# Optimization experiments

Hardware: AMD Instinct MI355X
Metric: run time of the kernel (lower is better)

## Reference

```python
import jax, jax.numpy as jnp
import numpy as np

WS = 8
HEADS = 12


def _dwconv(x, w, b):
    # x: (N, C, H, W); w: (C, 1, 3, 3) depthwise, zero pad 1
    y = jax.lax.conv_general_dilated(
        x, w, window_strides=(1, 1), padding=((1, 1), (1, 1)),
        dimension_numbers=("NCHW", "OIHW", "NCHW"), feature_group_count=x.shape[1])
    return y + b[None, :, None, None]


def _sepconv(x, dw, db, pw, pb):
    y = _dwconv(x, dw, db)
    # pointwise 1x1 conv: (N,C,H,W) x (O,C) -> (N,O,H,W)
    return jnp.einsum("nchw,oc->nohw", y, pw) + pb[None, :, None, None]


def _rel_pos_index(ws):
    coords = np.stack(np.meshgrid(np.arange(ws), np.arange(ws), indexing="ij"))  # (2, ws, ws)
    cf = coords.reshape(2, -1)
    rel = cf[:, :, None] - cf[:, None, :]          # (2, ws*ws, ws*ws)
    rel = rel.transpose(1, 2, 0).copy()
    rel[..., 0] += ws - 1
    rel[..., 1] += ws - 1
    rel[..., 0] *= 2 * ws - 1
    return rel.sum(-1)                             # (ws*ws, ws*ws)


def setup_inputs() -> dict:
    key = jax.random.key(0)
    ks = jax.random.split(key, 16)
    B, T, C, H, W = 2, 1, 384, 192, 192
    s = 0.02
    inp = {
        "vid": jax.random.normal(ks[0], (B, T, C, H, W), jnp.float32),
        "qd_w": jax.random.normal(ks[1], (C, 1, 3, 3), jnp.float32) * s,
        "qd_b": jnp.zeros((C,), jnp.float32),
        "qp_w": jax.random.normal(ks[2], (C, C), jnp.float32) * s,
        "qp_b": jnp.zeros((C,), jnp.float32),
        "kd_w": jax.random.normal(ks[3], (C, 1, 3, 3), jnp.float32) * s,
        "kd_b": jnp.zeros((C,), jnp.float32),
        "kp_w": jax.random.normal(ks[4], (C, C), jnp.float32) * s,
        "kp_b": jnp.zeros((C,), jnp.float32),
        "vd_w": jax.random.normal(ks[5], (C, 1, 3, 3), jnp.float32) * s,
        "vd_b": jnp.zeros((C,), jnp.float32),
        "vp_w": jax.random.normal(ks[6], (C, C), jnp.float32) * s,
        "vp_b": jnp.zeros((C,), jnp.float32),
        "rpb_table": jax.random.normal(ks[7], ((2 * WS - 1) ** 2, HEADS), jnp.float32) * s,
        "proj_w": jax.random.normal(ks[8], (C, C), jnp.float32) * s,
        "proj_b": jnp.zeros((C,), jnp.float32),
    }
    return inp


def reference(vid, qd_w, qd_b, qp_w, qp_b, kd_w, kd_b, kp_w, kp_b,
              vd_w, vd_b, vp_w, vp_b, rpb_table, proj_w, proj_b):
    B, T, C, H, W = vid.shape
    heads, ws = HEADS, WS
    hd = C // heads
    scale = hd ** -0.5
    x = vid.reshape(B * T, C, H, W)

    q = _sepconv(x, qd_w, qd_b, qp_w, qp_b) * scale
    k = _sepconv(x, kd_w, kd_b, kp_w, kp_b)
    v = _sepconv(x, vd_w, vd_b, vp_w, vp_b)

    nh, nw = H // ws, W // ws

    def win(z):  # (N, C, H, W) -> (N*nh*nw, heads, ws*ws, hd)
        N = z.shape[0]
        z = z.reshape(N, heads, hd, nh, ws, nw, ws)
        z = z.transpose(0, 3, 5, 1, 4, 6, 2)  # N, nh, nw, heads, ws, ws, hd
        return z.reshape(N * nh * nw, heads, ws * ws, hd)

    qw, kw, vw = win(q), win(k), win(v)

    # product search within window (dists = q . k), rel-pos bias softmax
    attn = jnp.einsum("nhqd,nhkd->nhqk", qw, kw)
    rp_idx = _rel_pos_index(ws)  # static (64, 64)
    bias = rpb_table[rp_idx.reshape(-1)].reshape(ws * ws, ws * ws, heads)
    bias = bias.transpose(2, 0, 1)  # (heads, 64, 64)
    attn = jax.nn.softmax(attn + bias[None], axis=-1)

    # weighted patch sum (ps=1 -> pixels)
    out = jnp.einsum("nhqk,nhkd->nhqd", attn, vw)  # (N*nh*nw, heads, ws*ws, hd)

    # un-window, merge heads into (h c) channel order, then token projection
    out = out.reshape(B * T, nh, nw, heads, ws, ws, hd)
    out = out.transpose(0, 1, 4, 2, 5, 3, 6).reshape(B * T, H, W, heads * hd)
    out = out @ proj_w.T + proj_b

    # fold (ps=1, stride0=1): identity overlap-add, zvid == 1
    out = out.transpose(0, 3, 1, 2).reshape(B, T, C, H, W)
    return out
```

## Files before the change

kernel.cpp:

```cpp
#include <hip/hip_runtime.h>

#define CCH 384
#define HH 192
#define WWD 192
#define NIMG 2
#define HWP (HH * WWD)
#define PTOT (NIMG * HWP)
#define HEADS 12
#define HD 32
#define NWIN 24
#define WINS 576
#define EELEM ((size_t)NIMG * CCH * HWP)
#define WMAT 147456

typedef __attribute__((ext_vector_type(8))) short bh8;
typedef __attribute__((ext_vector_type(8))) unsigned short us8;
typedef __attribute__((ext_vector_type(4))) unsigned short us4;
typedef __attribute__((ext_vector_type(4))) float fx4;

__device__ __forceinline__ unsigned short f2bf(float f) {
    unsigned u = __float_as_uint(f);
    u += 0x7fffu + ((u >> 16) & 1u);
    return (unsigned short)(u >> 16);
}

__device__ __forceinline__ void gload16(const void* g, void* l) {
    __builtin_amdgcn_global_load_lds(
        (const __attribute__((address_space(1))) void*)g,
        (__attribute__((address_space(3))) void*)l, 16, 0, 0);
}

__global__ __launch_bounds__(256) void prep(
    const float* __restrict__ qp, const float* __restrict__ kp,
    const float* __restrict__ vp, const float* __restrict__ pj,
    const float* __restrict__ qd, const float* __restrict__ kd,
    const float* __restrict__ vd, const float* __restrict__ rpb,
    unsigned short* __restrict__ Wb, float* __restrict__ dwT,
    float* __restrict__ Bx)
{
    int bx = blockIdx.x;
    if (bx < 288) {
        int idx8 = (bx * 256 + threadIdx.x) * 8;
        int which = idx8 / WMAT;
        int loc = idx8 - which * WMAT;
        const float* s = (which == 0) ? qp : (which == 1) ? kp : (which == 2) ? vp : pj;
        float4 v0 = *(const float4*)(s + loc);
        float4 v1 = *(const float4*)(s + loc + 4);
        us8 ov;
        ov[0] = f2bf(v0.x); ov[1] = f2bf(v0.y); ov[2] = f2bf(v0.z); ov[3] = f2bf(v0.w);
        ov[4] = f2bf(v1.x); ov[5] = f2bf(v1.y); ov[6] = f2bf(v1.z); ov[7] = f2bf(v1.w);
        *(us8*)(Wb + idx8) = ov;
    } else if (bx < 329) {
        int idx = (bx - 288) * 256 + threadIdx.x;
        if (idx < 3 * 9 * CCH) {
            int ten = idx / (9 * CCH);
            int rem = idx - ten * (9 * CCH);
            int tap = rem / CCH;
            int c   = rem - tap * CCH;
            const float* s = (ten == 0) ? qd : (ten == 1) ? kd : vd;
            dwT[idx] = s[c * 9 + tap];
        }
    } else {
        int idx = (bx - 329) * 256 + threadIdx.x;
        int h  = idx >> 12;
        int tk = (idx >> 6) & 63;
        int tq = idx & 63;
        int dy = (tq >> 3) - (tk >> 3) + 7;
        int dx = (tq & 7) - (tk & 7) + 7;
        Bx[idx] = rpb[(dy * 15 + dx) * HEADS + h];
    }
}

__global__ __launch_bounds__(256) void dwgather(
    const float* __restrict__ x,
    const float* __restrict__ wt,
    const float* __restrict__ qb, const float* __restrict__ kb,
    const float* __restrict__ vb,
    unsigned short* __restrict__ oq, unsigned short* __restrict__ ok,
    unsigned short* __restrict__ ov)
{
    __shared__ float halo[32 * 121];

    int bid = blockIdx.x;
    int b = (bid & 7) * 1728 + (bid >> 3);
    int wtx  = b % 24;
    int rest = b / 24;
    int chv  = rest % 12;
    int nwy  = rest / 12;
    int wy   = nwy % 24;
    int n    = nwy / 24;

    int h0 = wy * 8, w0 = wtx * 8;
    int tid = threadIdx.x;
    int c   = tid & 31;
    int pxg = tid >> 5;
    int cg  = chv * 32 + c;
    int widx = n * WINS + wy * NWIN + wtx;

    const float* xbase = x + (size_t)n * CCH * HWP + (size_t)(chv * 32) * HWP;

    for (int j = tid; j < 960; j += 256) {
        int seg = j % 3;
        int t   = j / 3;
        int rr  = t % 10;
        int cc  = t / 10;
        int hr  = h0 - 1 + rr;
        int cb  = w0 - 2 + seg * 4;
        float4 val = make_float4(0.f, 0.f, 0.f, 0.f);
        if (hr >= 0 && hr < HH) {
            const float* p = xbase + (size_t)cc * HWP + (size_t)hr * WWD;
            if (cb >= 0 && cb + 4 <= WWD) {
                val = *(const float4*)(p + cb);
            } else {
                if (cb + 0 >= 0 && cb + 0 < WWD) val.x = p[cb + 0];
                if (cb + 1 >= 0 && cb + 1 < WWD) val.y = p[cb + 1];
                if (cb + 2 >= 0 && cb + 2 < WWD) val.z = p[cb + 2];
                if (cb + 3 >= 0 && cb + 3 < WWD) val.w = p[cb + 3];
            }
        }
        int hb = cc * 121 + rr * 12 + seg * 4;
        halo[hb + 0] = val.x;
        halo[hb + 1] = val.y;
        halo[hb + 2] = val.z;
        halo[hb + 3] = val.w;
    }

    float wq[9], wk[9], wv[9];
#pragma unroll
    for (int t = 0; t < 9; ++t) {
        wq[t] = wt[t * CCH + cg];
        wk[t] = wt[9 * CCH + t * CCH + cg];
        wv[t] = wt[18 * CCH + t * CCH + cg];
    }
    float bqv = qb[cg], bkv = kb[cg], bvv = vb[cg];

    __syncthreads();

    const int hbase = c * 121 + pxg * 12;
    float r0[10], r1[10], r2[10];
#pragma unroll
    for (int cc = 0; cc < 10; ++cc) r0[cc] = halo[hbase + cc + 1];
#pragma unroll
    for (int cc = 0; cc < 10; ++cc) r1[cc] = halo[hbase + 12 + cc + 1];
#pragma unroll
    for (int cc = 0; cc < 10; ++cc) r2[cc] = halo[hbase + 24 + cc + 1];

    size_t ob0 = ((size_t)widx * 64 + pxg * 8) * CCH + cg;

#pragma unroll
    for (int pc = 0; pc < 8; ++pc) {
        float sq = 0.f, sk = 0.f, sv = 0.f;
#pragma unroll
        for (int dc = 0; dc < 3; ++dc) {
            float x0 = r0[pc + dc], x1 = r1[pc + dc], x2 = r2[pc + dc];
            sq = fmaf(x0, wq[dc], sq);     sk = fmaf(x0, wk[dc], sk);     sv = fmaf(x0, wv[dc], sv);
            sq = fmaf(x1, wq[3 + dc], sq); sk = fmaf(x1, wk[3 + dc], sk); sv = fmaf(x1, wv[3 + dc], sv);
            sq = fmaf(x2, wq[6 + dc], sq); sk = fmaf(x2, wk[6 + dc], sk); sv = fmaf(x2, wv[6 + dc], sv);
        }
        size_t o = ob0 + (size_t)pc * CCH;
        oq[o] = f2bf(sq + bqv);
        ok[o] = f2bf(sk + bkv);
        ov[o] = f2bf(sv + bvv);
    }
}

__global__ __launch_bounds__(256) void qkv_gemm(
    const unsigned short* __restrict__ tr0, const unsigned short* __restrict__ tr1,
    const unsigned short* __restrict__ tr2, const unsigned short* __restrict__ Wball,
    const float* __restrict__ qpb, const float* __restrict__ kpb,
    const float* __restrict__ vpb, float scale,
    unsigned short* __restrict__ qo, unsigned short* __restrict__ ko,
    unsigned short* __restrict__ vo)
{
    __shared__ __align__(16) char smem[33792];
    typedef unsigned short (*tile3)[128][32];
    tile3 Wt = (tile3)smem;
    tile3 Yt = (tile3)(smem + 16384);
    typedef unsigned short (*tep_t)[132];
    tep_t T16 = (tep_t)smem;

    int z = blockIdx.z;
    const unsigned short* Y  = (z == 0) ? tr0 : (z == 1) ? tr1 : tr2;
    const unsigned short* Wb = Wball + (size_t)z * WMAT;
    const float* bias        = (z == 0) ? qpb : (z == 1) ? kpb : vpb;
    float sc                 = (z == 0) ? scale : 1.0f;
    unsigned short* outb     = (z == 0) ? qo : (z == 1) ? ko : vo;
    bool vmode = (z == 2);

    int tid = threadIdx.x;
    int pp0 = blockIdx.x * 128;
    int cm0 = blockIdx.y * 128;
    int lid = tid & 63, wid = tid >> 6;
    int wr = wid >> 1, wc = wid & 1;
    int li = lid & 15, g = lid >> 4;

    int srow = (lid >> 2);
    int scol = (lid & 3) * 8;

    fx4 acc[4][4];
#pragma unroll
    for (int i = 0; i < 4; ++i)
#pragma unroll
        for (int j = 0; j < 4; ++j) acc[i][j] = (fx4){0.f, 0.f, 0.f, 0.f};

    tile3 A3 = vmode ? Yt : Wt;
    tile3 B3 = vmode ? Wt : Yt;

    const unsigned short* Wg0 = Wb + (size_t)(cm0 + wid * 32 + srow) * CCH + scol;
    const unsigned short* Yg0 = Y  + (size_t)(pp0 + wid * 32 + srow) * CCH + scol;

#pragma unroll
    for (int qi = 0; qi < 2; ++qi) {
        gload16(Wg0 + (size_t)qi * 16 * CCH, &Wt[0][wid * 32 + qi * 16][0]);
        gload16(Yg0 + (size_t)qi * 16 * CCH, &Yt[0][wid * 32 + qi * 16][0]);
    }
    __syncthreads();

    for (int kt = 0; kt < 12; ++kt) {
        int cur = kt & 1;
        if (kt < 11) {
            int k1 = (kt + 1) * 32;
#pragma unroll
            for (int qi = 0; qi < 2; ++qi) {
                gload16(Wg0 + (size_t)qi * 16 * CCH + k1, &Wt[cur ^ 1][wid * 32 + qi * 16][0]);
                gload16(Yg0 + (size_t)qi * 16 * CCH + k1, &Yt[cur ^ 1][wid * 32 + qi * 16][0]);
            }
        }

        bh8 a[4], b[4];
#pragma unroll
        for (int mf = 0; mf < 4; ++mf)
            a[mf] = *(const bh8*)&A3[cur][wr * 64 + mf * 16 + li][g * 8];
#pragma unroll
        for (int nf = 0; nf < 4; ++nf)
            b[nf] = *(const bh8*)&B3[cur][wc * 64 + nf * 16 + li][g * 8];
#pragma unroll
        for (int mf = 0; mf < 4; ++mf)
#pragma unroll
            for (int nf = 0; nf < 4; ++nf)
                acc[mf][nf] = __builtin_amdgcn_mfma_f32_16x16x32_bf16(
                    a[mf], b[nf], acc[mf][nf], 0, 0, 0);

        __syncthreads();
    }

    if (!vmode) {
#pragma unroll
        for (int mf = 0; mf < 4; ++mf) {
            int cl = wr * 64 + mf * 16 + g * 4;
            float4 bv = *(const float4*)&bias[cm0 + cl];
#pragma unroll
            for (int nf = 0; nf < 4; ++nf) {
                int pl = wc * 64 + nf * 16 + li;
                us4 o;
                o[0] = f2bf((acc[mf][nf][0] + bv.x) * sc);
                o[1] = f2bf((acc[mf][nf][1] + bv.y) * sc);
                o[2] = f2bf((acc[mf][nf][2] + bv.z) * sc);
                o[3] = f2bf((acc[mf][nf][3] + bv.w) * sc);
                *(us4*)&T16[pl][cl] = o;
            }
        }
        __syncthreads();
#pragma unroll
        for (int it = 0; it < 8; ++it) {
            int row = it * 16 + wid * 4 + (lid >> 4);
            int col = (lid & 15) * 8;
            us8 vv = *(const us8*)&T16[row][col];
            *(us8*)(outb + (size_t)(pp0 + row) * CCH + cm0 + col) = vv;
        }
    } else {
#pragma unroll
        for (int nf = 0; nf < 4; ++nf) {
            int cl = wc * 64 + nf * 16 + li;
            float bv = bias[cm0 + cl];
#pragma unroll
            for (int mf = 0; mf < 4; ++mf) {
                int pl = wr * 64 + mf * 16 + g * 4;
                us4 o;
                o[0] = f2bf(acc[mf][nf][0] + bv);
                o[1] = f2bf(acc[mf][nf][1] + bv);
                o[2] = f2bf(acc[mf][nf][2] + bv);
                o[3] = f2bf(acc[mf][nf][3] + bv);
                *(us4*)&T16[cl][pl] = o;
            }
        }
        __syncthreads();
        int n = pp0 / HWP;
        int pl0 = pp0 - n * HWP;
#pragma unroll
        for (int it = 0; it < 8; ++it) {
            int row = it * 16 + wid * 4 + (lid >> 4);
            int col = (lid & 15) * 8;
            us8 vv = *(const us8*)&T16[row][col];
            *(us8*)(outb + (size_t)(n * CCH + cm0 + row) * HWP + pl0 + col) = vv;
        }
    }
}

__global__ __launch_bounds__(256) void proj_gemm(
    const unsigned short* __restrict__ Y, const unsigned short* __restrict__ Wb,
    const float* __restrict__ bias, float* __restrict__ outf)
{
    __shared__ unsigned short Wt[2][128][32];
    __shared__ unsigned short Yt[2][128][32];

    int tid = threadIdx.x;
    int pp0 = blockIdx.x * 128;
    int cm0 = blockIdx.y * 128;
    int lid = tid & 63, wid = tid >> 6;
    int wr = wid >> 1, wc = wid & 1;
    int li = lid & 15, g = lid >> 4;

    int srow = (lid >> 2);
    int scol = (lid & 3) * 8;

    fx4 acc[4][4];
#pragma unroll
    for (int i = 0; i < 4; ++i)
#pragma unroll
        for (int j = 0; j < 4; ++j) acc[i][j] = (fx4){0.f, 0.f, 0.f, 0.f};

    const unsigned short* Wg0 = Wb + (size_t)(cm0 + wid * 32 + srow) * CCH + scol;
    const unsigned short* Yg0 = Y  + (size_t)(pp0 + wid * 32 + srow) * CCH + scol;

#pragma unroll
    for (int qi = 0; qi < 2; ++qi) {
        gload16(Wg0 + (size_t)qi * 16 * CCH, &Wt[0][wid * 32 + qi * 16][0]);
        gload16(Yg0 + (size_t)qi * 16 * CCH, &Yt[0][wid * 32 + qi * 16][0]);
    }
    __syncthreads();

    for (int kt = 0; kt < 12; ++kt) {
        int cur = kt & 1;
        if (kt < 11) {
            int k1 = (kt + 1) * 32;
#pragma unroll
            for (int qi = 0; qi < 2; ++qi) {
                gload16(Wg0 + (size_t)qi * 16 * CCH + k1, &Wt[cur ^ 1][wid * 32 + qi * 16][0]);
                gload16(Yg0 + (size_t)qi * 16 * CCH + k1, &Yt[cur ^ 1][wid * 32 + qi * 16][0]);
            }
        }

        bh8 a[4], b[4];
#pragma unroll
        for (int mf = 0; mf < 4; ++mf)
            a[mf] = *(const bh8*)&Wt[cur][wr * 64 + mf * 16 + li][g * 8];
#pragma unroll
        for (int nf = 0; nf < 4; ++nf)
            b[nf] = *(const bh8*)&Yt[cur][wc * 64 + nf * 16 + li][g * 8];
#pragma unroll
        for (int mf = 0; mf < 4; ++mf)
#pragma unroll
            for (int nf = 0; nf < 4; ++nf)
                acc[mf][nf] = __builtin_amdgcn_mfma_f32_16x16x32_bf16(
                    a[mf], b[nf], acc[mf][nf], 0, 0, 0);

        __syncthreads();
    }

#pragma unroll
    for (int mf = 0; mf < 4; ++mf) {
        int c = cm0 + wr * 64 + mf * 16 + g * 4;
#pragma unroll
        for (int nf = 0; nf < 4; ++nf) {
            int p = pp0 + wc * 64 + nf * 16 + li;
            int n = p / HWP;
            int rem = p - n * HWP;
            int win = rem >> 6, t = rem & 63;
            int h = (win / NWIN) * 8 + (t >> 3);
            int w = (win % NWIN) * 8 + (t & 7);
            float* op = outf + (size_t)n * CCH * HWP + (size_t)h * WWD + w;
#pragma unroll
            for (int r = 0; r < 4; ++r)
                op[(size_t)(c + r) * HWP] = acc[mf][nf][r] + bias[c + r];
        }
    }
}

__global__ __launch_bounds__(256) void attn(
    const unsigned short* __restrict__ q, const unsigned short* __restrict__ k,
    const unsigned short* __restrict__ v, const float* __restrict__ Bx,
    unsigned short* __restrict__ o)
{
    __shared__ unsigned short Pl[4][64][72];

    int tid = threadIdx.x, lid = tid & 63, wid = tid >> 6;
    int wl = blockIdx.x;
    int n = wl / WINS, winl = wl - n * WINS;
    int li = lid & 15, g = lid >> 4;

    const fx4 z = (fx4){0.f, 0.f, 0.f, 0.f};

    for (int hq = wid; hq < HEADS; hq += 4) {
        const unsigned short* qp = q + (size_t)(wl * 64) * CCH + hq * HD + g * 8;
        const unsigned short* kp = k + (size_t)(wl * 64) * CCH + hq * HD + g * 8;
        bh8 aq[4], bk[4];
#pragma unroll
        for (int mf = 0; mf < 4; ++mf)
            aq[mf] = *(const bh8*)(qp + (size_t)(mf * 16 + li) * CCH);
#pragma unroll
        for (int nf = 0; nf < 4; ++nf)
            bk[nf] = *(const bh8*)(kp + (size_t)(nf * 16 + li) * CCH);

        fx4 s[4][4];
#pragma unroll
        for (int mf = 0; mf < 4; ++mf)
#pragma unroll
            for (int nf = 0; nf < 4; ++nf)
                s[mf][nf] = __builtin_amdgcn_mfma_f32_16x16x32_bf16(aq[mf], bk[nf], z, 0, 0, 0);

#pragma unroll
        for (int mf = 0; mf < 4; ++mf)
#pragma unroll
            for (int nf = 0; nf < 4; ++nf) {
                fx4 bv = *(const fx4*)&Bx[((size_t)hq * 64 + nf * 16 + li) * 64
                                          + mf * 16 + g * 4];
                s[mf][nf] += bv;
            }

        float inv_[4][4];
#pragma unroll
        for (int mf = 0; mf < 4; ++mf)
#pragma unroll
            for (int r = 0; r < 4; ++r) {
                float m = s[mf][0][r];
#pragma unroll
                for (int nf = 1; nf < 4; ++nf) m = fmaxf(m, s[mf][nf][r]);
                m = fmaxf(m, __shfl_xor(m, 1));
                m = fmaxf(m, __shfl_xor(m, 2));
                m = fmaxf(m, __shfl_xor(m, 4));
                m = fmaxf(m, __shfl_xor(m, 8));
                float sum = 0.f;
#pragma unroll
                for (int nf = 0; nf < 4; ++nf) {
                    float e = __expf(s[mf][nf][r] - m);
                    s[mf][nf][r] = e;
                    sum += e;
                }
                sum += __shfl_xor(sum, 1);
                sum += __shfl_xor(sum, 2);
                sum += __shfl_xor(sum, 4);
                sum += __shfl_xor(sum, 8);
                inv_[mf][r] = 1.f / sum;
            }

#pragma unroll
        for (int mf = 0; mf < 4; ++mf)
#pragma unroll
            for (int nf = 0; nf < 4; ++nf)
#pragma unroll
                for (int r = 0; r < 4; ++r)
                    Pl[wid][mf * 16 + g * 4 + r][nf * 16 + li] =
                        f2bf(s[mf][nf][r] * inv_[mf][r]);

        fx4 o2[2][4];
#pragma unroll
        for (int m2 = 0; m2 < 2; ++m2)
#pragma unroll
            for (int nf = 0; nf < 4; ++nf) o2[m2][nf] = z;
#pragma unroll
        for (int ks = 0; ks < 2; ++ks) {
            bh8 av[2], bp[4];
#pragma unroll
            for (int m2 = 0; m2 < 2; ++m2)
                av[m2] = *(const bh8*)(v + (size_t)(n * CCH + hq * HD + m2 * 16 + li) * HWP
                                         + winl * 64 + ks * 32 + g * 8);
#pragma unroll
            for (int nf = 0; nf < 4; ++nf)
                bp[nf] = *(const bh8*)&Pl[wid][nf * 16 + li][ks * 32 + g * 8];
#pragma unroll
            for (int m2 = 0; m2 < 2; ++m2)
#pragma unroll
                for (int nf = 0; nf < 4; ++nf)
                    o2[m2][nf] = __builtin_amdgcn_mfma_f32_16x16x32_bf16(
                        av[m2], bp[nf], o2[m2][nf], 0, 0, 0);
        }
#pragma unroll
        for (int nf = 0; nf < 4; ++nf) {
            int tq = nf * 16 + li;
#pragma unroll
            for (int m2 = 0; m2 < 2; ++m2) {
                int d = hq * HD + m2 * 16 + g * 4;
                us4 ov;
                ov[0] = f2bf(o2[m2][nf][0]);
                ov[1] = f2bf(o2[m2][nf][1]);
                ov[2] = f2bf(o2[m2][nf][2]);
                ov[3] = f2bf(o2[m2][nf][3]);
                *(us4*)(o + (size_t)(wl * 64 + tq) * CCH + d) = ov;
            }
        }
    }
}

extern "C" void kernel_launch(void* const* d_in, const int* in_sizes, int n_in,
                              void* d_out, int out_size, void* d_ws, size_t ws_size,
                              hipStream_t stream) {
    const float* vid  = (const float*)d_in[0];
    const float* qd_w = (const float*)d_in[1];
    const float* qd_b = (const float*)d_in[2];
    const float* qp_w = (const float*)d_in[3];
    const float* qp_b = (const float*)d_in[4];
    const float* kd_w = (const float*)d_in[5];
    const float* kd_b = (const float*)d_in[6];
    const float* kp_w = (const float*)d_in[7];
    const float* kp_b = (const float*)d_in[8];
    const float* vd_w = (const float*)d_in[9];
    const float* vd_b = (const float*)d_in[10];
    const float* vp_w = (const float*)d_in[11];
    const float* vp_b = (const float*)d_in[12];
    const float* rpb  = (const float*)d_in[13];
    const float* pj_w = (const float*)d_in[14];
    const float* pj_b = (const float*)d_in[15];

    unsigned short* ws16 = (unsigned short*)d_ws;
    unsigned short* tr0 = ws16 + 3 * EELEM;
    unsigned short* tr1 = ws16 + 4 * EELEM;
    unsigned short* tr2 = ws16 + 5 * EELEM;
    unsigned short* Wb  = ws16 + 6 * EELEM;
    float* dwT          = (float*)(Wb + 4 * WMAT);
    float* Bx           = dwT + 3 * 9 * CCH;
    unsigned short* qb  = ws16;
    unsigned short* kb  = ws16 + EELEM;
    unsigned short* vb  = ws16 + 2 * EELEM;
    unsigned short* ob  = tr0;

    prep<<<521, 256, 0, stream>>>(qp_w, kp_w, vp_w, pj_w,
                                  qd_w, kd_w, vd_w, rpb, Wb, dwT, Bx);
    dwgather<<<NIMG * WINS * 12, 256, 0, stream>>>(
        vid, dwT, qd_b, kd_b, vd_b, tr0, tr1, tr2);

    const float scale = 0.17677669529663687f;
    qkv_gemm<<<dim3(PTOT / 128, 3, 3), 256, 0, stream>>>(
        tr0, tr1, tr2, Wb, qp_b, kp_b, vp_b, scale, qb, kb, vb);

    attn<<<NIMG * WINS, 256, 0, stream>>>(qb, kb, vb, Bx, ob);

    proj_gemm<<<dim3(PTOT / 128, 3), 256, 0, stream>>>(
        ob, Wb + 3 * WMAT, pj_b, (float*)d_out);
}
```

Baseline: 420.6 us.

## Widen dwconv tiles to 64 channels and swizzle GEMM LDS with XCD-aware block order

The depthwise-conv gather kernel now handles 64 channels per block and two pixel rows per thread. It reuses the loaded halo rows for the second row, which halves the block count and cuts redundant LDS reads. The QKV and projection GEMMs move to a 1D grid with a block-index remap that interleaves blocks across the 8 XCDs. They also XOR-swizzle the LDS column layout to reduce bank conflicts on MFMA fragment loads. The larger halo buffer raises LDS use per block, and the remap changes L2 locality in ways that are hard to predict.

```diff
diff --git a/kernel.cpp b/kernel.cpp
--- a/kernel.cpp
+++ b/kernel.cpp
@@ -79,27 +79,27 @@
     unsigned short* __restrict__ oq, unsigned short* __restrict__ ok,
     unsigned short* __restrict__ ov)
 {
-    __shared__ float halo[32 * 121];
+    __shared__ float halo[64 * 121];
 
     int bid = blockIdx.x;
-    int b = (bid & 7) * 1728 + (bid >> 3);
+    int b = (bid & 7) * 864 + (bid >> 3);
     int wtx  = b % 24;
-    int rest = b / 24;
-    int chv  = rest % 12;
-    int nwy  = rest / 12;
+    int strip = b / 24;
+    int chv  = strip % 6;
+    int nwy  = strip / 6;
     int wy   = nwy % 24;
     int n    = nwy / 24;
 
     int h0 = wy * 8, w0 = wtx * 8;
     int tid = threadIdx.x;
-    int c   = tid & 31;
-    int pxg = tid >> 5;
-    int cg  = chv * 32 + c;
+    int c   = tid & 63;
+    int pxg = tid >> 6;
+    int cg  = chv * 64 + c;
     int widx = n * WINS + wy * NWIN + wtx;
 
-    const float* xbase = x + (size_t)n * CCH * HWP + (size_t)(chv * 32) * HWP;
-
-    for (int j = tid; j < 960; j += 256) {
+    const float* xbase = x + (size_t)n * CCH * HWP + (size_t)(chv * 64) * HWP;
+
+    for (int j = tid; j < 1920; j += 256) {
         int seg = j % 3;
         int t   = j / 3;
         int rr  = t % 10;
@@ -136,7 +136,7 @@
 
     __syncthreads();
 
-    const int hbase = c * 121 + pxg * 12;
+    const int hbase = c * 121 + (2 * pxg) * 12;
     float r0[10], r1[10], r2[10];
 #pragma unroll
     for (int cc = 0; cc < 10; ++cc) r0[cc] = halo[hbase + cc + 1];
@@ -145,7 +145,7 @@
 #pragma unroll
     for (int cc = 0; cc < 10; ++cc) r2[cc] = halo[hbase + 24 + cc + 1];
 
-    size_t ob0 = ((size_t)widx * 64 + pxg * 8) * CCH + cg;
+    size_t ob0 = ((size_t)widx * 64 + pxg * 16) * CCH + cg;
 
 #pragma unroll
     for (int pc = 0; pc < 8; ++pc) {
@@ -158,6 +158,25 @@
             sq = fmaf(x2, wq[6 + dc], sq); sk = fmaf(x2, wk[6 + dc], sk); sv = fmaf(x2, wv[6 + dc], sv);
         }
         size_t o = ob0 + (size_t)pc * CCH;
+        oq[o] = f2bf(sq + bqv);
+        ok[o] = f2bf(sk + bkv);
+        ov[o] = f2bf(sv + bvv);
+    }
+
+#pragma unroll
+    for (int cc = 0; cc < 10; ++cc) r0[cc] = halo[hbase + 36 + cc + 1];
+
+#pragma unroll
+    for (int pc = 0; pc < 8; ++pc) {
+        float sq = 0.f, sk = 0.f, sv = 0.f;
+#pragma unroll
+        for (int dc = 0; dc < 3; ++dc) {
+            float x0 = r1[pc + dc], x1 = r2[pc + dc], x2 = r0[pc + dc];
+            sq = fmaf(x0, wq[dc], sq);     sk = fmaf(x0, wk[dc], sk);     sv = fmaf(x0, wv[dc], sv);
+            sq = fmaf(x1, wq[3 + dc], sq); sk = fmaf(x1, wk[3 + dc], sk); sv = fmaf(x1, wv[3 + dc], sv);
+            sq = fmaf(x2, wq[6 + dc], sq); sk = fmaf(x2, wk[6 + dc], sk); sv = fmaf(x2, wv[6 + dc], sv);
+        }
+        size_t o = ob0 + (size_t)(8 + pc) * CCH;
         oq[o] = f2bf(sq + bqv);
         ok[o] = f2bf(sk + bkv);
         ov[o] = f2bf(sv + bvv);
@@ -179,7 +198,14 @@
     typedef unsigned short (*tep_t)[132];
     tep_t T16 = (tep_t)smem;
 
-    int z = blockIdx.z;
+    int bL = blockIdx.x;
+    int O  = (bL & 7) * 648 + (bL >> 3);
+    int z  = O / 1728;
+    int rem = O - z * 1728;
+    int py = rem / 3;
+    int cx = rem - py * 3;
+    int pp0 = py * 128, cm0 = cx * 128;
+
     const unsigned short* Y  = (z == 0) ? tr0 : (z == 1) ? tr1 : tr2;
     const unsigned short* Wb = Wball + (size_t)z * WMAT;
     const float* bias        = (z == 0) ? qpb : (z == 1) ? kpb : vpb;
@@ -188,14 +214,13 @@
     bool vmode = (z == 2);
 
     int tid = threadIdx.x;
-    int pp0 = blockIdx.x * 128;
-    int cm0 = blockIdx.y * 128;
     int lid = tid & 63, wid = tid >> 6;
     int wr = wid >> 1, wc = wid & 1;
     int li = lid & 15, g = lid >> 4;
 
     int srow = (lid >> 2);
-    int scol = (lid & 3) * 8;
+    int scol = (((lid & 3) ^ ((srow >> 1) & 3))) * 8;
+    int gsw = (g ^ ((li >> 1) & 3)) * 8;
 
     fx4 acc[4][4];
 #pragma unroll
@@ -230,10 +255,10 @@
         bh8 a[4], b[4];
 #pragma unroll
         for (int mf = 0; mf < 4; ++mf)
-            a[mf] = *(const bh8*)&A3[cur][wr * 64 + mf * 16 + li][g * 8];
+            a[mf] = *(const bh8*)&A3[cur][wr * 64 + mf * 16 + li][gsw];
 #pragma unroll
         for (int nf = 0; nf < 4; ++nf)
-            b[nf] = *(const bh8*)&B3[cur][wc * 64 + nf * 16 + li][g * 8];
+            b[nf] = *(const bh8*)&B3[cur][wc * 64 + nf * 16 + li][gsw];
 #pragma unroll
         for (int mf = 0; mf < 4; ++mf)
 #pragma unroll
@@ -304,15 +329,20 @@
     __shared__ unsigned short Wt[2][128][32];
     __shared__ unsigned short Yt[2][128][32];
 
+    int bL = blockIdx.x;
+    int O  = (bL & 7) * 216 + (bL >> 3);
+    int py = O / 3;
+    int cx = O - py * 3;
+    int pp0 = py * 128, cm0 = cx * 128;
+
     int tid = threadIdx.x;
-    int pp0 = blockIdx.x * 128;
-    int cm0 = blockIdx.y * 128;
     int lid = tid & 63, wid = tid >> 6;
     int wr = wid >> 1, wc = wid & 1;
     int li = lid & 15, g = lid >> 4;
 
     int srow = (lid >> 2);
-    int scol = (lid & 3) * 8;
+    int scol = (((lid & 3) ^ ((srow >> 1) & 3))) * 8;
+    int gsw = (g ^ ((li >> 1) & 3)) * 8;
 
     fx4 acc[4][4];
 #pragma unroll
@@ -344,10 +374,10 @@
         bh8 a[4], b[4];
 #pragma unroll
         for (int mf = 0; mf < 4; ++mf)
-            a[mf] = *(const bh8*)&Wt[cur][wr * 64 + mf * 16 + li][g * 8];
+            a[mf] = *(const bh8*)&Wt[cur][wr * 64 + mf * 16 + li][gsw];
 #pragma unroll
         for (int nf = 0; nf < 4; ++nf)
-            b[nf] = *(const bh8*)&Yt[cur][wc * 64 + nf * 16 + li][g * 8];
+            b[nf] = *(const bh8*)&Yt[cur][wc * 64 + nf * 16 + li][gsw];
 #pragma unroll
         for (int mf = 0; mf < 4; ++mf)
 #pragma unroll
@@ -526,15 +556,15 @@
 
     prep<<<521, 256, 0, stream>>>(qp_w, kp_w, vp_w, pj_w,
                                   qd_w, kd_w, vd_w, rpb, Wb, dwT, Bx);
-    dwgather<<<NIMG * WINS * 12, 256, 0, stream>>>(
+    dwgather<<<NIMG * WINS * 6, 256, 0, stream>>>(
         vid, dwT, qd_b, kd_b, vd_b, tr0, tr1, tr2);
 
     const float scale = 0.17677669529663687f;
-    qkv_gemm<<<dim3(PTOT / 128, 3, 3), 256, 0, stream>>>(
+    qkv_gemm<<<5184, 256, 0, stream>>>(
         tr0, tr1, tr2, Wb, qp_b, kp_b, vp_b, scale, qb, kb, vb);
 
     attn<<<NIMG * WINS, 256, 0, stream>>>(qb, kb, vb, Bx, ob);
 
-    proj_gemm<<<dim3(PTOT / 128, 3), 256, 0, stream>>>(
+    proj_gemm<<<1728, 256, 0, stream>>>(
         ob, Wb + 3 * WMAT, pj_b, (float*)d_out);
 }
```

Measured after the change: 395.2 us. 6.0% less time.
